# Performance work log

Hardware: AMD Instinct MI355X
Metric: run time of the kernel (lower is better)

Reference implementation:

```python
import jax, jax.numpy as jnp
import numpy as np

L, D, H, DK, DV, VOCAB, PAD = 6, 512, 8, 64, 64, 10000, 0
B, S, NR = 32, 64, 196

def setup_inputs() -> dict:
    key = jax.random.key(0)
    ks = jax.random.split(key, 16)
    sd = 0.02
    emb = jax.random.normal(ks[0], (VOCAB, D), jnp.float32) * sd
    emb = emb.at[PAD].set(0.0)  # padding_idx row is zero in torch Embedding
    def w(k, shape):
        return jax.random.normal(k, shape, jnp.float32) * sd
    return {
        "x": jax.random.randint(ks[1], (B, S), 0, VOCAB),
        "K": jax.random.normal(ks[2], (B, NR, D), jnp.float32),
        "V": jax.random.normal(ks[3], (B, NR, D), jnp.float32),
        "g": jax.random.normal(ks[4], (B, D), jnp.float32),
        "batch_size": B,
        "emb": emb,
        "Wq_s": w(ks[5], (L, D, H * DK)),
        "Wk_s": w(ks[6], (L, D, H * DK)),
        "Wv_s": w(ks[7], (L, D, H * DV)),
        "Wo_s": w(ks[8], (L, H * DV, D)),
        "Wq_c": w(ks[9], (L, D, H * DK)),
        "Wg_c": w(ks[10], (L, D, H * DK)),
        "Wk_c": w(ks[11], (L, D, H * DK)),
        "Wv_c": w(ks[12], (L, D, H * DV)),
        "Wo_c": w(ks[13], (L, H * DV, D)),
        "Wf": w(ks[14], (D, VOCAB)),
        "bf": jnp.zeros((VOCAB,), jnp.float32),
    }

def positional_encoding(seq_len, d_model):
    pos = jnp.arange(seq_len, dtype=jnp.float32)[:, None]          # [S,1]
    j = jnp.arange(d_model // 2, dtype=jnp.float32)[None, :]       # [1,D/2]
    ang = pos / jnp.power(10000.0, 2.0 * j / d_model)              # [S,D/2]
    pe = jnp.stack([jnp.sin(ang), jnp.cos(ang)], axis=-1)          # [S,D/2,2]
    return pe.reshape(seq_len, d_model)

def attend(q, k, v, mask):
    # q:[B,Sq,H,DK] k:[B,Sk,H,DK] v:[B,Sk,H,DV]
    scores = jnp.einsum('bqhd,bkhd->bhqk', q, k) / jnp.sqrt(jnp.float32(DK))
    if mask is not None:
        scores = jnp.where(mask[None, None], scores, jnp.finfo(scores.dtype).min)
    attn = jax.nn.softmax(scores, axis=-1)
    return jnp.einsum('bhqk,bkhd->bqhd', attn, v)

def reference(x, K, V, g, batch_size, emb, Wq_s, Wk_s, Wv_s, Wo_s,
              Wq_c, Wg_c, Wk_c, Wv_c, Wo_c, Wf, bf):
    b, s = x.shape
    out = emb[x] + positional_encoding(s, D)[None]                 # [B,S,D]
    mask = jnp.tril(jnp.ones((s, s), bool))                        # causal: True = attend
    for l in range(L):
        # masked multi-head self-attention
        q = (out @ Wq_s[l]).reshape(b, s, H, DK)
        k = (out @ Wk_s[l]).reshape(b, s, H, DK)
        v = (out @ Wv_s[l]).reshape(b, s, H, DV)
        out = attend(q, k, v, mask).reshape(b, s, H * DV) @ Wo_s[l]
        # global-adaptive cross-attention: query conditioned on global feature g
        q = (out @ Wq_c[l] + (g @ Wg_c[l])[:, None, :]).reshape(b, s, H, DK)
        kk = (K @ Wk_c[l]).reshape(b, NR, H, DK)
        vv = (V @ Wv_c[l]).reshape(b, NR, H, DV)
        out = attend(q, kk, vv, None).reshape(b, s, H * DV) @ Wo_c[l]
    return jax.nn.softmax(out @ Wf + bf, axis=-1)                  # [B,S,VOCAB]
```

## Files before the change

kernel.cpp:

```cpp
#include <hip/hip_runtime.h>
#include <math.h>


#define S2 (512*512)
typedef unsigned short ushort_t;
typedef unsigned int u32;
typedef __attribute__((ext_vector_type(8))) short short8;
typedef __attribute__((ext_vector_type(4))) float f32x4;

__device__ __forceinline__ ushort_t f2b(float f) {
    union { float f; u32 u; } v; v.f = f;
    u32 r = (v.u + 0x7fffu + ((v.u >> 16) & 1u)) >> 16;
    return (ushort_t)r;
}
__device__ __forceinline__ float b2f(ushort_t u) {
    union { u32 u; float f; } v; v.u = ((u32)u) << 16; return v.f;
}
__device__ __forceinline__ void glds16(const void* g, void* l) {
    __builtin_amdgcn_global_load_lds((const __attribute__((address_space(1))) u32*)g,
                                     (__attribute__((address_space(3))) u32*)l,
                                     16, 0, 0);
}
__device__ __forceinline__ f32x4 mfma16(short8 a, short8 b, f32x4 c) {
    return __builtin_amdgcn_mfma_f32_16x16x32_bf16(a, b, c, 0, 0, 0);
}

__device__ __forceinline__ void tile128(
    const ushort_t* __restrict__ A, const ushort_t* __restrict__ B,
    ushort_t* __restrict__ Cp, int N, int K, const float* __restrict__ biasc,
    int m0, int n0, ushort_t* As, ushort_t* Bs, ushort_t* Cs)
{
    int t = threadIdx.x;
    int sr = t >> 2, sk = (t & 3) * 8;
    int wv = t >> 6, lane = t & 63;
    int wr = (wv >> 1) * 64, wc = (wv & 1) * 64;
    int lr = lane & 15, lq = lane >> 4;

    f32x4 acc[4][4];
#pragma unroll
    for (int i = 0; i < 4; ++i)
#pragma unroll
        for (int j = 0; j < 4; ++j) acc[i][j] = (f32x4){0.f, 0.f, 0.f, 0.f};

    for (int k0 = 0; k0 < K; k0 += 32) {
        glds16(A + (long)(m0 + sr) * K + k0 + sk,      (void*)(As + t * 8));
        glds16(A + (long)(m0 + sr + 64) * K + k0 + sk, (void*)(As + (t + 256) * 8));
        glds16(B + (long)(n0 + sr) * K + k0 + sk,      (void*)(Bs + t * 8));
        glds16(B + (long)(n0 + sr + 64) * K + k0 + sk, (void*)(Bs + (t + 256) * 8));
        __syncthreads();
        short8 af[4], bfr[4];
#pragma unroll
        for (int i = 0; i < 4; ++i)
            af[i] = *(const short8*)&As[(wr + i * 16 + lr) * 32 + lq * 8];
#pragma unroll
        for (int j = 0; j < 4; ++j)
            bfr[j] = *(const short8*)&Bs[(wc + j * 16 + lr) * 32 + lq * 8];
#pragma unroll
        for (int i = 0; i < 4; ++i)
#pragma unroll
            for (int j = 0; j < 4; ++j)
                acc[i][j] = mfma16(af[i], bfr[j], acc[i][j]);
        __syncthreads();
    }

    ushort_t* Cw = Cs + wv * 16 * 80;
#pragma unroll
    for (int i = 0; i < 4; ++i) {
#pragma unroll
        for (int j = 0; j < 4; ++j) {
            int colg = n0 + wc + j * 16 + lr;
            float bb = (biasc && colg < N) ? biasc[colg] : 0.f;
#pragma unroll
            for (int r = 0; r < 4; ++r)
                Cw[(lq * 4 + r) * 80 + j * 16 + lr] = f2b(acc[i][j][r] + bb);
        }
        __syncthreads();
#pragma unroll
        for (int rr = 0; rr < 2; ++rr) {
            int c = lane + 64 * rr;
            int row = c >> 3, g8 = c & 7;
            uint4 u = *(const uint4*)&Cw[row * 80 + g8 * 8];
            int colg = n0 + wc + g8 * 8;
            int rowg = m0 + wr + i * 16 + row;
            if (colg < N) *(uint4*)&Cp[(long)rowg * N + colg] = u;
        }
        __syncthreads();
    }
}

__global__ __launch_bounds__(256) void gemm_bt(
    const ushort_t* __restrict__ A, const ushort_t* __restrict__ B,
    ushort_t* __restrict__ C, int N, int K, const float* __restrict__ biasc)
{
    __shared__ ushort_t As[128 * 32], Bs[128 * 32];
    __shared__ __align__(16) ushort_t Cs[4 * 16 * 80];
    tile128(A, B, C, N, K, biasc, blockIdx.y * 128, blockIdx.x * 128, As, Bs, Cs);
}

__global__ __launch_bounds__(256) void fusew(
    const ushort_t* __restrict__ W8t, const ushort_t* __restrict__ Wo_sp,
    const ushort_t* __restrict__ Wo_cp, ushort_t* __restrict__ Fqc_t,
    ushort_t* __restrict__ Fqkv_t)
{
    __shared__ ushort_t As[128 * 32], Bs[128 * 32];
    __shared__ __align__(16) ushort_t Cs[4 * 16 * 80];
    int z = blockIdx.z;
    const ushort_t *A, *B; ushort_t* C;
    if (z < 6)      { A = W8t + (long)(24 + z) * S2; B = Wo_sp + (long)z * S2; C = Fqc_t + (long)z * S2; }
    else { int zz = z - 6, l = zz / 3, m = zz % 3;
           A = W8t + (long)(m * 6 + l + 1) * S2; B = Wo_cp + (long)l * S2; C = Fqkv_t + (long)zz * S2; }
    tile128(A, B, C, 512, 512, nullptr, blockIdx.y * 128, blockIdx.x * 128, As, Bs, Cs);
}

__global__ __launch_bounds__(256) void kcv_gemm(
    const ushort_t* __restrict__ Kb, const ushort_t* __restrict__ Vb,
    const ushort_t* __restrict__ W8t, ushort_t* __restrict__ kcv)
{
    __shared__ ushort_t As[128 * 32], Bs[128 * 32];
    __shared__ __align__(16) ushort_t Cs[4 * 16 * 80];
    int z = blockIdx.z, l = z >> 1, isv = z & 1;
    const ushort_t* A = isv ? Vb : Kb;
    const ushort_t* B = W8t + (long)(30 + isv * 6 + l) * S2;
    ushort_t* C = kcv + (long)z * 3211264;
    tile128(A, B, C, 512, 512, nullptr, blockIdx.y * 128, blockIdx.x * 128, As, Bs, Cs);
}

__global__ __launch_bounds__(256) void prep(
    const int* __restrict__ x, const float* __restrict__ emb,
    const float* __restrict__ Wq_s, const float* __restrict__ Wk_s,
    const float* __restrict__ Wv_s, const float* __restrict__ Wo_s,
    const float* __restrict__ Wq_c, const float* __restrict__ Wg_c,
    const float* __restrict__ Wk_c, const float* __restrict__ Wv_c,
    const float* __restrict__ Wo_c, const float* __restrict__ Wf,
    const float* __restrict__ Kin, const float* __restrict__ Vin,
    const float* __restrict__ g,
    ushort_t* __restrict__ W8t, ushort_t* __restrict__ Wf_t,
    ushort_t* __restrict__ Wo_sp, ushort_t* __restrict__ Wo_cp,
    ushort_t* __restrict__ K_bf, ushort_t* __restrict__ V_bf,
    ushort_t* __restrict__ act0, float* __restrict__ gq)
{
    __shared__ float tile[2][64][65];
    int bid = blockIdx.x, t = threadIdx.x;
    if (bid < 1536) {
        int mat = bid >> 5, wsel = mat / 6, l = mat % 6;
        const float* src = (wsel == 0) ? Wq_s : (wsel == 1) ? Wk_s : (wsel == 2) ? Wv_s :
                           (wsel == 3) ? Wo_s : (wsel == 4) ? Wq_c : (wsel == 5) ? Wk_c :
                           (wsel == 6) ? Wv_c : Wo_c;
        src += (long)l * S2;
        ushort_t* dst = W8t + (long)mat * S2;
        ushort_t* plain = (wsel == 3) ? Wo_sp + (long)l * S2
                        : (wsel == 7) ? Wo_cp + (long)l * S2 : nullptr;
        int within = bid & 31;
        int n0 = (within & 7) * 64, kb = (within >> 3) * 128;
        int r0 = t >> 4, c4 = (t & 15) * 4;
        float4 v[2][4];
#pragma unroll
        for (int h2 = 0; h2 < 2; ++h2)
#pragma unroll
            for (int p = 0; p < 4; ++p)
                v[h2][p] = *(const float4*)(src + (long)(kb + h2 * 64 + p * 16 + r0) * 512 + n0 + c4);
#pragma unroll
        for (int h2 = 0; h2 < 2; ++h2)
#pragma unroll
            for (int p = 0; p < 4; ++p) {
                int r = p * 16 + r0;
                tile[h2][c4 + 0][r] = v[h2][p].x; tile[h2][c4 + 1][r] = v[h2][p].y;
                tile[h2][c4 + 2][r] = v[h2][p].z; tile[h2][c4 + 3][r] = v[h2][p].w;
            }
        if (plain) {
#pragma unroll
            for (int h2 = 0; h2 < 2; ++h2)
#pragma unroll
                for (int p = 0; p < 4; ++p) {
                    ushort4 w;
                    w.x = f2b(v[h2][p].x); w.y = f2b(v[h2][p].y);
                    w.z = f2b(v[h2][p].z); w.w = f2b(v[h2][p].w);
                    *(ushort4*)(plain + (long)(kb + h2 * 64 + p * 16 + r0) * 512 + n0 + c4) = w;
                }
        }
        __syncthreads();
#pragma unroll
        for (int h2 = 0; h2 < 2; ++h2)
#pragma unroll
            for (int q = 0; q < 2; ++q) {
                int nl = q * 32 + (t >> 3), k8 = (t & 7) * 8;
                short8 o;
#pragma unroll
                for (int u = 0; u < 8; ++u) o[u] = (short)f2b(tile[h2][nl][k8 + u]);
                *(short8*)(dst + (long)(n0 + nl) * 512 + kb + h2 * 64 + k8) = o;
            }
    } else if (bid < 2168) {
        int id = bid - 1536;
        int n0 = (id % 158) * 64, kb = (id / 158) * 128;
        int r0 = t >> 4, c4 = (t & 15) * 4;
        int n = n0 + c4;
        float4 v[2][4];
#pragma unroll
        for (int h2 = 0; h2 < 2; ++h2)
#pragma unroll
            for (int p = 0; p < 4; ++p) {
                const float* row = Wf + (long)(kb + h2 * 64 + p * 16 + r0) * 10000;
                float4 w;
                if (n + 3 < 10000) {
                    w = *(const float4*)(row + n);
                } else {
                    w.x = (n + 0 < 10000) ? row[n + 0] : 0.f;
                    w.y = (n + 1 < 10000) ? row[n + 1] : 0.f;
                    w.z = (n + 2 < 10000) ? row[n + 2] : 0.f;
                    w.w = (n + 3 < 10000) ? row[n + 3] : 0.f;
                }
                v[h2][p] = w;
            }
#pragma unroll
        for (int h2 = 0; h2 < 2; ++h2)
#pragma unroll
            for (int p = 0; p < 4; ++p) {
                int r = p * 16 + r0;
                tile[h2][c4 + 0][r] = v[h2][p].x; tile[h2][c4 + 1][r] = v[h2][p].y;
                tile[h2][c4 + 2][r] = v[h2][p].z; tile[h2][c4 + 3][r] = v[h2][p].w;
            }
        __syncthreads();
#pragma unroll
        for (int h2 = 0; h2 < 2; ++h2)
#pragma unroll
            for (int q = 0; q < 2; ++q) {
                int nl = q * 32 + (t >> 3), k8 = (t & 7) * 8;
                short8 o;
#pragma unroll
                for (int u = 0; u < 8; ++u) o[u] = (short)f2b(tile[h2][nl][k8 + u]);
                *(short8*)(Wf_t + (long)(n0 + nl) * 512 + kb + h2 * 64 + k8) = o;
            }
    } else if (bid < 2952) {
        int sec = bid - 2168;
        const float* s; ushort_t* o; long fbase;
        if (sec < 392) { s = Kin; o = K_bf; fbase = (long)sec * 2048; }
        else           { s = Vin; o = V_bf; fbase = (long)(sec - 392) * 2048; }
        float4 v[8];
#pragma unroll
        for (int u = 0; u < 8; ++u)
            v[u] = *(const float4*)(s + 4 * (fbase + t + 256 * u));
#pragma unroll
        for (int u = 0; u < 8; ++u) {
            long fi = fbase + t + 256 * u;
            ushort4 w;
            w.x = f2b(v[u].x); w.y = f2b(v[u].y); w.z = f2b(v[u].z); w.w = f2b(v[u].w);
            *(ushort4*)(o + 4 * fi) = w;
        }
    } else if (bid < 3464) {
        long i = (long)(bid - 2952) * 2048 + t * 8;
        long tok = i >> 9;
        int d8 = (int)(i & 511);
        int s = (int)(tok & 63);
        int id = x[tok];
        const float* erow = emb + (long)id * 512 + d8;
        float4 e0 = *(const float4*)(erow);
        float4 e1 = *(const float4*)(erow + 4);
        float ev[8] = {e0.x, e0.y, e0.z, e0.w, e1.x, e1.y, e1.z, e1.w};
        int j0 = d8 >> 1;
        float sf = (float)s;
        short8 o;
#pragma unroll
        for (int u = 0; u < 4; ++u) {
            float invf = expf(-0.035977892f * (float)(j0 + u));
            float ang = sf * invf;
            o[2 * u]     = (short)f2b(ev[2 * u]     + sinf(ang));
            o[2 * u + 1] = (short)f2b(ev[2 * u + 1] + cosf(ang));
        }
        *(short8*)(act0 + i) = o;
    } else {
        __shared__ float gs[512];
        int id = bid - 3464;
        int lb = id >> 1, half = id & 1;
        int l = lb >> 5, b = lb & 31;
        for (int i = t; i < 512; i += 256) gs[i] = g[b * 512 + i];
        __syncthreads();
        int o = half * 256 + t;
        const float* wcol = Wg_c + (long)l * S2 + o;
        float acc = 0.f;
#pragma unroll 8
        for (int i = 0; i < 512; ++i) acc += gs[i] * wcol[(long)i * 512];
        gq[((long)l * 32 + b) * 512 + o] = acc;
    }
}

__global__ __launch_bounds__(256, 1) void layer_self(
    const ushort_t* __restrict__ act,
    const ushort_t* __restrict__ Wq, const ushort_t* __restrict__ Wk,
    const ushort_t* __restrict__ Wv, ushort_t* __restrict__ attnout)
{
    __shared__ __align__(16) char smem[111616];
    ushort_t* Wst = (ushort_t*)smem;
    ushort_t* Qs  = (ushort_t*)(smem + 66560);
    ushort_t* Ks  = (ushort_t*)(smem + 75776);
    ushort_t* Vt  = (ushort_t*)(smem + 84992);
    float*    Ss  = (float*)(smem + 94208);

    int b = blockIdx.x >> 3, h = blockIdx.x & 7;
    int t = threadIdx.x, wv = t >> 6, lane = t & 63;
    int lr = lane & 15, lq = lane >> 4;
    const ushort_t* actb = act + (long)b * 64 * 512;

    for (int mat = 0; mat < 3; ++mat) {
        const ushort_t* W = ((mat == 0) ? Wq : (mat == 1) ? Wk : Wv) + h * 64 * 512;
        __syncthreads();
#pragma unroll
        for (int i = 0; i < 16; ++i) {
            int row = i * 4 + wv;
            glds16(W + row * 512 + lane * 8, Wst + row * 520 + lane * 8);
        }
        __syncthreads();
        f32x4 acc[4];
#pragma unroll
        for (int j = 0; j < 4; ++j) acc[j] = (f32x4){0.f, 0.f, 0.f, 0.f};
        const ushort_t* arow = actb + (wv * 16 + lr) * 512;
#pragma unroll 4
        for (int k = 0; k < 16; ++k) {
            short8 a = *(const short8*)(arow + k * 32 + lq * 8);
#pragma unroll
            for (int j = 0; j < 4; ++j) {
                short8 bb = *(const short8*)&Wst[(j * 16 + lr) * 520 + k * 32 + lq * 8];
                acc[j] = mfma16(a, bb, acc[j]);
            }
        }
        if (mat == 2) {
#pragma unroll
            for (int j = 0; j < 4; ++j)
#pragma unroll
                for (int r = 0; r < 4; ++r)
                    Vt[(j * 16 + lr) * 72 + wv * 16 + lq * 4 + r] = f2b(acc[j][r]);
        } else {
            ushort_t* Dst = (mat == 0) ? Qs : Ks;
#pragma unroll
            for (int j = 0; j < 4; ++j)
#pragma unroll
                for (int r = 0; r < 4; ++r)
                    Dst[(wv * 16 + lq * 4 + r) * 72 + j * 16 + lr] = f2b(acc[j][r]);
        }
    }
    __syncthreads();

    f32x4 sc[4];
#pragma unroll
    for (int j = 0; j < 4; ++j) sc[j] = (f32x4){0.f, 0.f, 0.f, 0.f};
#pragma unroll
    for (int k2 = 0; k2 < 2; ++k2) {
        short8 a = *(const short8*)&Qs[(wv * 16 + lr) * 72 + k2 * 32 + lq * 8];
#pragma unroll
        for (int j = 0; j < 4; ++j) {
            short8 bb = *(const short8*)&Ks[(j * 16 + lr) * 72 + k2 * 32 + lq * 8];
            sc[j] = mfma16(a, bb, sc[j]);
        }
    }
#pragma unroll
    for (int j = 0; j < 4; ++j)
#pragma unroll
        for (int r = 0; r < 4; ++r)
            Ss[(wv * 16 + lq * 4 + r) * 68 + j * 16 + lr] = sc[j][r];
    __syncthreads();

    for (int rr = 0; rr < 16; ++rr) {
        int r = wv * 16 + rr;
        float sv = (lane <= r) ? Ss[r * 68 + lane] * 0.125f : -INFINITY;
        float m = sv;
        for (int off = 32; off; off >>= 1) m = fmaxf(m, __shfl_xor(m, off));
        float p = __expf(sv - m);
        float su = p;
        for (int off = 32; off; off >>= 1) su += __shfl_xor(su, off);
        Qs[r * 72 + lane] = f2b(p / su);
    }
    __syncthreads();

    f32x4 ov[4];
#pragma unroll
    for (int j = 0; j < 4; ++j) ov[j] = (f32x4){0.f, 0.f, 0.f, 0.f};
#pragma unroll
    for (int k2 = 0; k2 < 2; ++k2) {
        short8 a = *(const short8*)&Qs[(wv * 16 + lr) * 72 + k2 * 32 + lq * 8];
#pragma unroll
        for (int j = 0; j < 4; ++j) {
            short8 bb = *(const short8*)&Vt[(j * 16 + lr) * 72 + k2 * 32 + lq * 8];
            ov[j] = mfma16(a, bb, ov[j]);
        }
    }
    long obase = ((long)b * 64) * 512 + h * 64;
#pragma unroll
    for (int j = 0; j < 4; ++j)
#pragma unroll
        for (int r = 0; r < 4; ++r)
            attnout[obase + (long)(wv * 16 + lq * 4 + r) * 512 + j * 16 + lr] = f2b(ov[j][r]);
}

__global__ __launch_bounds__(256, 1) void layer_cross(
    const ushort_t* __restrict__ attnout, const ushort_t* __restrict__ Kb,
    const ushort_t* __restrict__ Vb, const ushort_t* __restrict__ Fqc,
    const ushort_t* __restrict__ Wkc, const ushort_t* __restrict__ Wvc,
    const float* __restrict__ gql, ushort_t* __restrict__ crossout)
{
    __shared__ __align__(16) char smem[134400];
    ushort_t* Wst = (ushort_t*)smem;
    float*    Ss  = (float*)smem;
    ushort_t* Qs  = (ushort_t*)(smem + 66560);
    ushort_t* Kc  = (ushort_t*)(smem + 75776);
    ushort_t* Pb  = Kc;
    ushort_t* Vt  = (ushort_t*)(smem + 105728);

    int b = blockIdx.x >> 3, h = blockIdx.x & 7;
    int t = threadIdx.x, wv = t >> 6, lane = t & 63;
    int lr = lane & 15, lq = lane >> 4;
    const ushort_t* atb = attnout + (long)b * 64 * 512;
    const ushort_t* Kbb = Kb + (long)b * 196 * 512;
    const ushort_t* Vbb = Vb + (long)b * 196 * 512;

    {
        const ushort_t* W = Fqc + h * 64 * 512;
#pragma unroll
        for (int i = 0; i < 16; ++i) {
            int row = i * 4 + wv;
            glds16(W + row * 512 + lane * 8, Wst + row * 520 + lane * 8);
        }
        __syncthreads();
        f32x4 acc[4];
#pragma unroll
        for (int j = 0; j < 4; ++j) acc[j] = (f32x4){0.f, 0.f, 0.f, 0.f};
        const ushort_t* arow = atb + (wv * 16 + lr) * 512;
#pragma unroll 4
        for (int k = 0; k < 16; ++k) {
            short8 a = *(const short8*)(arow + k * 32 + lq * 8);
#pragma unroll
            for (int j = 0; j < 4; ++j) {
                short8 bb = *(const short8*)&Wst[(j * 16 + lr) * 520 + k * 32 + lq * 8];
                acc[j] = mfma16(a, bb, acc[j]);
            }
        }
#pragma unroll
        for (int j = 0; j < 4; ++j)
#pragma unroll
            for (int r = 0; r < 4; ++r) {
                int col = j * 16 + lr;
                Qs[(wv * 16 + lq * 4 + r) * 72 + col] =
                    f2b(acc[j][r] + gql[b * 512 + h * 64 + col]);
            }
    }
#pragma unroll
    for (int mat = 0; mat < 2; ++mat) {
        const ushort_t* W = ((mat == 0) ? Wkc : Wvc) + h * 64 * 512;
        const ushort_t* Src = (mat == 0) ? Kbb : Vbb;
        __syncthreads();
#pragma unroll
        for (int i = 0; i < 16; ++i) {
            int row = i * 4 + wv;
            glds16(W + row * 512 + lane * 8, Wst + row * 520 + lane * 8);
        }
        __syncthreads();
        for (int rt = wv; rt < 13; rt += 4) {
            f32x4 acc[4];
#pragma unroll
            for (int j = 0; j < 4; ++j) acc[j] = (f32x4){0.f, 0.f, 0.f, 0.f};
            const ushort_t* arow = Src + (long)(rt * 16 + lr) * 512;
#pragma unroll 4
            for (int k = 0; k < 16; ++k) {
                short8 a = *(const short8*)(arow + k * 32 + lq * 8);
#pragma unroll
                for (int j = 0; j < 4; ++j) {
                    short8 bb = *(const short8*)&Wst[(j * 16 + lr) * 520 + k * 32 + lq * 8];
                    acc[j] = mfma16(a, bb, acc[j]);
                }
            }
            if (mat == 0) {
#pragma unroll
                for (int j = 0; j < 4; ++j)
#pragma unroll
                    for (int r = 0; r < 4; ++r)
                        Kc[(rt * 16 + lq * 4 + r) * 72 + j * 16 + lr] = f2b(acc[j][r]);
            } else {
#pragma unroll
                for (int j = 0; j < 4; ++j)
#pragma unroll
                    for (int r = 0; r < 4; ++r)
                        Vt[(j * 16 + lr) * 224 + rt * 16 + lq * 4 + r] = f2b(acc[j][r]);
            }
        }
    }
    __syncthreads();
    for (int e = t; e < 64 * 28; e += 256) Vt[(e / 28) * 224 + 196 + (e % 28)] = 0;

    f32x4 sc[13];
#pragma unroll
    for (int ct = 0; ct < 13; ++ct) sc[ct] = (f32x4){0.f, 0.f, 0.f, 0.f};
#pragma unroll
    for (int k2 = 0; k2 < 2; ++k2) {
        short8 a = *(const short8*)&Qs[(wv * 16 + lr) * 72 + k2 * 32 + lq * 8];
#pragma unroll
        for (int ct = 0; ct < 13; ++ct) {
            short8 bb = *(const short8*)&Kc[(ct * 16 + lr) * 72 + k2 * 32 + lq * 8];
            sc[ct] = mfma16(a, bb, sc[ct]);
        }
    }
#pragma unroll
    for (int ct = 0; ct < 13; ++ct)
#pragma unroll
        for (int r = 0; r < 4; ++r)
            Ss[(wv * 16 + lq * 4 + r) * 216 + ct * 16 + lr] = sc[ct][r];
    __syncthreads();

    for (int rr = 0; rr < 16; ++rr) {
        int r = wv * 16 + rr;
        float v0 = Ss[r * 216 + lane] * 0.125f;
        float v1 = Ss[r * 216 + 64 + lane] * 0.125f;
        float v2 = Ss[r * 216 + 128 + lane] * 0.125f;
        float v3 = (lane < 4) ? Ss[r * 216 + 192 + lane] * 0.125f : -INFINITY;
        float m = fmaxf(fmaxf(v0, v1), fmaxf(v2, v3));
        for (int off = 32; off; off >>= 1) m = fmaxf(m, __shfl_xor(m, off));
        float e0 = __expf(v0 - m), e1 = __expf(v1 - m), e2 = __expf(v2 - m);
        float e3 = (lane < 4) ? __expf(v3 - m) : 0.f;
        float su = e0 + e1 + e2 + e3;
        for (int off = 32; off; off >>= 1) su += __shfl_xor(su, off);
        float inv = 1.f / su;
        Pb[r * 224 + lane]       = f2b(e0 * inv);
        Pb[r * 224 + 64 + lane]  = f2b(e1 * inv);
        Pb[r * 224 + 128 + lane] = f2b(e2 * inv);
        if (lane < 4)  Pb[r * 224 + 192 + lane] = f2b(e3 * inv);
        if (lane < 28) Pb[r * 224 + 196 + lane] = 0;
    }
    __syncthreads();

    f32x4 ov[4];
#pragma unroll
    for (int j = 0; j < 4; ++j) ov[j] = (f32x4){0.f, 0.f, 0.f, 0.f};
#pragma unroll
    for (int k2 = 0; k2 < 7; ++k2) {
        short8 a = *(const short8*)&Pb[(wv * 16 + lr) * 224 + k2 * 32 + lq * 8];
#pragma unroll
        for (int j = 0; j < 4; ++j) {
            short8 bb = *(const short8*)&Vt[(j * 16 + lr) * 224 + k2 * 32 + lq * 8];
            ov[j] = mfma16(a, bb, ov[j]);
        }
    }
    long obase = ((long)b * 64) * 512 + h * 64;
#pragma unroll
    for (int j = 0; j < 4; ++j)
#pragma unroll
        for (int r = 0; r < 4; ++r)
            crossout[obase + (long)(wv * 16 + lq * 4 + r) * 512 + j * 16 + lr] = f2b(ov[j][r]);
}

__global__ __launch_bounds__(256, 1) void layer_cross_pre(
    const ushort_t* __restrict__ attnout, const ushort_t* __restrict__ kcl,
    const ushort_t* __restrict__ vcl, const ushort_t* __restrict__ Fqc,
    const float* __restrict__ gql, ushort_t* __restrict__ crossout)
{
    __shared__ __align__(16) char smem[134400];
    ushort_t* Wst = (ushort_t*)smem;
    float*    Ss  = (float*)smem;
    ushort_t* Qs  = (ushort_t*)(smem + 66560);
    ushort_t* Kc  = (ushort_t*)(smem + 75776);
    ushort_t* Pb  = Kc;
    ushort_t* Vt  = (ushort_t*)(smem + 105728);

    int b = blockIdx.x >> 3, h = blockIdx.x & 7;
    int t = threadIdx.x, wv = t >> 6, lane = t & 63;
    int lr = lane & 15, lq = lane >> 4;
    const ushort_t* atb = attnout + (long)b * 64 * 512;

    {
        const ushort_t* W = Fqc + h * 64 * 512;
#pragma unroll
        for (int i = 0; i < 16; ++i) {
            int row = i * 4 + wv;
            glds16(W + row * 512 + lane * 8, Wst + row * 520 + lane * 8);
        }
        __syncthreads();
        f32x4 acc[4];
#pragma unroll
        for (int j = 0; j < 4; ++j) acc[j] = (f32x4){0.f, 0.f, 0.f, 0.f};
        const ushort_t* arow = atb + (wv * 16 + lr) * 512;
#pragma unroll 4
        for (int k = 0; k < 16; ++k) {
            short8 a = *(const short8*)(arow + k * 32 + lq * 8);
#pragma unroll
            for (int j = 0; j < 4; ++j) {
                short8 bb = *(const short8*)&Wst[(j * 16 + lr) * 520 + k * 32 + lq * 8];
                acc[j] = mfma16(a, bb, acc[j]);
            }
        }
#pragma unroll
        for (int j = 0; j < 4; ++j)
#pragma unroll
            for (int r = 0; r < 4; ++r) {
                int col = j * 16 + lr;
                Qs[(wv * 16 + lq * 4 + r) * 72 + col] =
                    f2b(acc[j][r] + gql[b * 512 + h * 64 + col]);
            }
    }

    {
        const ushort_t* kr = kcl + ((long)b * 196) * 512 + h * 64;
        for (int idx = t; idx < 208 * 8; idx += 256) {
            int key = idx >> 3, d8 = (idx & 7) * 8;
            short8 v = (short8){0, 0, 0, 0, 0, 0, 0, 0};
            if (key < 196) v = *(const short8*)(kr + (long)key * 512 + d8);
            *(short8*)&Kc[key * 72 + d8] = v;
        }
        const ushort_t* vrp = vcl + ((long)b * 196) * 512 + h * 64;
        for (int idx = t; idx < 196 * 8; idx += 256) {
            int key = idx >> 3, d8 = (idx & 7) * 8;
            short8 v = *(const short8*)(vrp + (long)key * 512 + d8);
#pragma unroll
            for (int u = 0; u < 8; ++u) Vt[(d8 + u) * 224 + key] = v[u];
        }
        for (int e = t; e < 64 * 28; e += 256) Vt[(e / 28) * 224 + 196 + (e % 28)] = 0;
    }
    __syncthreads();

    f32x4 sc[13];
#pragma unroll
    for (int ct = 0; ct < 13; ++ct) sc[ct] = (f32x4){0.f, 0.f, 0.f, 0.f};
#pragma unroll
    for (int k2 = 0; k2 < 2; ++k2) {
        short8 a = *(const short8*)&Qs[(wv * 16 + lr) * 72 + k2 * 32 + lq * 8];
#pragma unroll
        for (int ct = 0; ct < 13; ++ct) {
            short8 bb = *(const short8*)&Kc[(ct * 16 + lr) * 72 + k2 * 32 + lq * 8];
            sc[ct] = mfma16(a, bb, sc[ct]);
        }
    }
#pragma unroll
    for (int ct = 0; ct < 13; ++ct)
#pragma unroll
        for (int r = 0; r < 4; ++r)
            Ss[(wv * 16 + lq * 4 + r) * 216 + ct * 16 + lr] = sc[ct][r];
    __syncthreads();

    for (int rr = 0; rr < 16; ++rr) {
        int r = wv * 16 + rr;
        float v0 = Ss[r * 216 + lane] * 0.125f;
        float v1 = Ss[r * 216 + 64 + lane] * 0.125f;
        float v2 = Ss[r * 216 + 128 + lane] * 0.125f;
        float v3 = (lane < 4) ? Ss[r * 216 + 192 + lane] * 0.125f : -INFINITY;
        float m = fmaxf(fmaxf(v0, v1), fmaxf(v2, v3));
        for (int off = 32; off; off >>= 1) m = fmaxf(m, __shfl_xor(m, off));
        float e0 = __expf(v0 - m), e1 = __expf(v1 - m), e2 = __expf(v2 - m);
        float e3 = (lane < 4) ? __expf(v3 - m) : 0.f;
        float su = e0 + e1 + e2 + e3;
        for (int off = 32; off; off >>= 1) su += __shfl_xor(su, off);
        float inv = 1.f / su;
        Pb[r * 224 + lane]       = f2b(e0 * inv);
        Pb[r * 224 + 64 + lane]  = f2b(e1 * inv);
        Pb[r * 224 + 128 + lane] = f2b(e2 * inv);
        if (lane < 4)  Pb[r * 224 + 192 + lane] = f2b(e3 * inv);
        if (lane < 28) Pb[r * 224 + 196 + lane] = 0;
    }
    __syncthreads();

    f32x4 ov[4];
#pragma unroll
    for (int j = 0; j < 4; ++j) ov[j] = (f32x4){0.f, 0.f, 0.f, 0.f};
#pragma unroll
    for (int k2 = 0; k2 < 7; ++k2) {
        short8 a = *(const short8*)&Pb[(wv * 16 + lr) * 224 + k2 * 32 + lq * 8];
#pragma unroll
        for (int j = 0; j < 4; ++j) {
            short8 bb = *(const short8*)&Vt[(j * 16 + lr) * 224 + k2 * 32 + lq * 8];
            ov[j] = mfma16(a, bb, ov[j]);
        }
    }
    long obase = ((long)b * 64) * 512 + h * 64;
#pragma unroll
    for (int j = 0; j < 4; ++j)
#pragma unroll
        for (int r = 0; r < 4; ++r)
            crossout[obase + (long)(wv * 16 + lq * 4 + r) * 512 + j * 16 + lr] = f2b(ov[j][r]);
}

__global__ __launch_bounds__(256) void softmax_bf(const ushort_t* __restrict__ lg,
                                                  float* __restrict__ out)
{
    __shared__ float red[8];
    long row = blockIdx.x;
    const ushort_t* p = lg + row * 10000L;
    float* po = out + row * 10000L;
    int t = threadIdx.x;
    int w = t >> 6, lane = t & 63;
    float vals[40];
    float mx = -INFINITY;
#pragma unroll
    for (int i = 0; i < 5; ++i) {
        int vi = t + (i << 8);
        if (vi < 1250) {
            short8 v = *(const short8*)(p + vi * 8);
#pragma unroll
            for (int u = 0; u < 8; ++u) {
                float f = b2f((ushort_t)v[u]);
                vals[i * 8 + u] = f;
                mx = fmaxf(mx, f);
            }
        } else {
#pragma unroll
            for (int u = 0; u < 8; ++u) vals[i * 8 + u] = -INFINITY;
        }
    }
    for (int off = 32; off; off >>= 1) mx = fmaxf(mx, __shfl_xor(mx, off));
    if (lane == 0) red[w] = mx;
    __syncthreads();
    mx = fmaxf(fmaxf(red[0], red[1]), fmaxf(red[2], red[3]));
    float s = 0.f;
#pragma unroll
    for (int ii = 0; ii < 40; ++ii) {
        float e = __expf(vals[ii] - mx);
        vals[ii] = e;
        s += e;
    }
    for (int off = 32; off; off >>= 1) s += __shfl_xor(s, off);
    if (lane == 0) red[4 + w] = s;
    __syncthreads();
    s = red[4] + red[5] + red[6] + red[7];
    float inv = 1.0f / s;
#pragma unroll
    for (int i = 0; i < 5; ++i) {
        int vi = t + (i << 8);
        if (vi < 1250) {
#pragma unroll
            for (int u4 = 0; u4 < 2; ++u4) {
                float4 o;
                o.x = vals[i * 8 + u4 * 4 + 0] * inv;
                o.y = vals[i * 8 + u4 * 4 + 1] * inv;
                o.z = vals[i * 8 + u4 * 4 + 2] * inv;
                o.w = vals[i * 8 + u4 * 4 + 3] * inv;
                *(float4*)(po + vi * 8 + u4 * 4) = o;
            }
        }
    }
}

extern "C" void kernel_launch(void* const* d_in, const int* in_sizes, int n_in,
                              void* d_out, int out_size, void* d_ws, size_t ws_size,
                              hipStream_t stream)
{
    const int*   x    = (const int*)d_in[0];
    const float* Kin  = (const float*)d_in[1];
    const float* Vin  = (const float*)d_in[2];
    const float* g    = (const float*)d_in[3];
    const float* emb  = (const float*)d_in[5];
    const float* Wq_s = (const float*)d_in[6];
    const float* Wk_s = (const float*)d_in[7];
    const float* Wv_s = (const float*)d_in[8];
    const float* Wo_s = (const float*)d_in[9];
    const float* Wq_c = (const float*)d_in[10];
    const float* Wg_c = (const float*)d_in[11];
    const float* Wk_c = (const float*)d_in[12];
    const float* Wv_c = (const float*)d_in[13];
    const float* Wo_c = (const float*)d_in[14];
    const float* Wf   = (const float*)d_in[15];
    const float* bf   = (const float*)d_in[16];
    float* out = (float*)d_out;

    float* gq = (float*)d_ws;
    ushort_t* act0     = (ushort_t*)(gq + 98304);
    ushort_t* crossout = act0 + 1048576;
    ushort_t* attnout  = crossout + 1048576;
    ushort_t* K_bf     = attnout + 1048576;
    ushort_t* V_bf     = K_bf + 3211264;
    ushort_t* W8t      = V_bf + 3211264;
    ushort_t* Wf_t     = W8t + 48L * S2;
    ushort_t* Wo_sp    = Wf_t + 5177344;
    ushort_t* Wo_cp    = Wo_sp + 6L * S2;
    ushort_t* Fqc_t    = Wo_cp + 6L * S2;
    ushort_t* Fqkv_t   = Fqc_t + 6L * S2;
    ushort_t* Wfin_t   = Fqkv_t + 15L * S2;
    ushort_t* kcv      = Wfin_t + 5177344;
    ushort_t* logits   = W8t;

    int use_pre = (ws_size >= 159776768ULL) ? 1 : 0;

    prep<<<3848, 256, 0, stream>>>(x, emb, Wq_s, Wk_s, Wv_s, Wo_s, Wq_c, Wg_c,
                                   Wk_c, Wv_c, Wo_c, Wf, Kin, Vin, g,
                                   W8t, Wf_t, Wo_sp, Wo_cp, K_bf, V_bf, act0, gq);
    fusew<<<dim3(4, 4, 21), 256, 0, stream>>>(W8t, Wo_sp, Wo_cp, Fqc_t, Fqkv_t);
    gemm_bt<<<dim3(4, 79, 1), 256, 0, stream>>>(Wf_t, Wo_cp + 5L * S2, Wfin_t,
                                                512, 512, nullptr);
    if (use_pre)
        kcv_gemm<<<dim3(4, 49, 12), 256, 0, stream>>>(K_bf, V_bf, W8t, kcv);

    for (int l = 0; l < 6; ++l) {
        const ushort_t *A, *Bq, *Bk, *Bv;
        if (l == 0) {
            A = act0;
            Bq = W8t + 0L * 6 * S2; Bk = W8t + 1L * 6 * S2; Bv = W8t + 2L * 6 * S2;
        } else {
            A = crossout;
            Bq = Fqkv_t + (long)((l - 1) * 3) * S2;
            Bk = Bq + S2; Bv = Bq + 2 * S2;
        }
        layer_self<<<256, 256, 0, stream>>>(A, Bq, Bk, Bv, attnout);
        if (use_pre)
            layer_cross_pre<<<256, 256, 0, stream>>>(attnout,
                                                     kcv + (long)(l * 2) * 3211264,
                                                     kcv + (long)(l * 2 + 1) * 3211264,
                                                     Fqc_t + (long)l * S2,
                                                     gq + (long)l * 16384, crossout);
        else
            layer_cross<<<256, 256, 0, stream>>>(attnout, K_bf, V_bf,
                                                 Fqc_t + (long)l * S2,
                                                 W8t + (long)(5 * 6 + l) * S2,
                                                 W8t + (long)(6 * 6 + l) * S2,
                                                 gq + (long)l * 16384, crossout);
    }

    gemm_bt<<<dim3(79, 16, 1), 256, 0, stream>>>(crossout, Wfin_t, logits,
                                                 10000, 512, bf);
    softmax_bf<<<2048, 256, 0, stream>>>(logits, out);
}
```

Before: 655.1 us.

## Read weights directly from global and do softmax in registers to raise occupancy

Removes the LDS staging of the per-head weight slice in the self-attention and cross-attention pre kernels, so the B operand is read straight from global memory. The score tile is no longer spilled to a float LDS buffer; softmax runs on the MFMA accumulators using 16-lane shuffles. This shrinks shared memory enough to allow two blocks per CU (launch bounds raised to 2) and drops several barriers. The cost is uncoalesced, cache-dependent global reads of the weights inside the MFMA loop and more register pressure from the register-resident softmax.

```diff
diff --git a/kernel.cpp b/kernel.cpp
--- a/kernel.cpp
+++ b/kernel.cpp
@@ -283,42 +283,34 @@
     }
 }
 
-__global__ __launch_bounds__(256, 1) void layer_self(
+__global__ __launch_bounds__(256, 2) void layer_self(
     const ushort_t* __restrict__ act,
     const ushort_t* __restrict__ Wq, const ushort_t* __restrict__ Wk,
     const ushort_t* __restrict__ Wv, ushort_t* __restrict__ attnout)
 {
-    __shared__ __align__(16) char smem[111616];
-    ushort_t* Wst = (ushort_t*)smem;
-    ushort_t* Qs  = (ushort_t*)(smem + 66560);
-    ushort_t* Ks  = (ushort_t*)(smem + 75776);
-    ushort_t* Vt  = (ushort_t*)(smem + 84992);
-    float*    Ss  = (float*)(smem + 94208);
+    __shared__ __align__(16) char smem[27648];
+    ushort_t* Qs = (ushort_t*)smem;
+    ushort_t* Ks = (ushort_t*)(smem + 9216);
+    ushort_t* Vt = (ushort_t*)(smem + 18432);
 
     int b = blockIdx.x >> 3, h = blockIdx.x & 7;
     int t = threadIdx.x, wv = t >> 6, lane = t & 63;
     int lr = lane & 15, lq = lane >> 4;
     const ushort_t* actb = act + (long)b * 64 * 512;
-
+    const ushort_t* arow = actb + (wv * 16 + lr) * 512;
+
+#pragma unroll
     for (int mat = 0; mat < 3; ++mat) {
         const ushort_t* W = ((mat == 0) ? Wq : (mat == 1) ? Wk : Wv) + h * 64 * 512;
-        __syncthreads();
-#pragma unroll
-        for (int i = 0; i < 16; ++i) {
-            int row = i * 4 + wv;
-            glds16(W + row * 512 + lane * 8, Wst + row * 520 + lane * 8);
-        }
-        __syncthreads();
         f32x4 acc[4];
 #pragma unroll
         for (int j = 0; j < 4; ++j) acc[j] = (f32x4){0.f, 0.f, 0.f, 0.f};
-        const ushort_t* arow = actb + (wv * 16 + lr) * 512;
 #pragma unroll 4
         for (int k = 0; k < 16; ++k) {
             short8 a = *(const short8*)(arow + k * 32 + lq * 8);
 #pragma unroll
             for (int j = 0; j < 4; ++j) {
-                short8 bb = *(const short8*)&Wst[(j * 16 + lr) * 520 + k * 32 + lq * 8];
+                short8 bb = *(const short8*)(W + (j * 16 + lr) * 512 + k * 32 + lq * 8);
                 acc[j] = mfma16(a, bb, acc[j]);
             }
         }
@@ -351,25 +343,26 @@
             sc[j] = mfma16(a, bb, sc[j]);
         }
     }
-#pragma unroll
-    for (int j = 0; j < 4; ++j)
-#pragma unroll
-        for (int r = 0; r < 4; ++r)
-            Ss[(wv * 16 + lq * 4 + r) * 68 + j * 16 + lr] = sc[j][r];
-    __syncthreads();
-
-    for (int rr = 0; rr < 16; ++rr) {
-        int r = wv * 16 + rr;
-        float sv = (lane <= r) ? Ss[r * 68 + lane] * 0.125f : -INFINITY;
-        float m = sv;
-        for (int off = 32; off; off >>= 1) m = fmaxf(m, __shfl_xor(m, off));
-        float p = __expf(sv - m);
-        float su = p;
-        for (int off = 32; off; off >>= 1) su += __shfl_xor(su, off);
-        Qs[r * 72 + lane] = f2b(p / su);
-    }
-    __syncthreads();
-
+
+#pragma unroll
+    for (int r = 0; r < 4; ++r) {
+        int row = wv * 16 + lq * 4 + r;
+        float v[4], m = -INFINITY;
+#pragma unroll
+        for (int j = 0; j < 4; ++j) {
+            v[j] = (j * 16 + lr <= row) ? sc[j][r] * 0.125f : -INFINITY;
+            m = fmaxf(m, v[j]);
+        }
+        for (int off = 8; off; off >>= 1) m = fmaxf(m, __shfl_xor(m, off));
+        float su = 0.f;
+#pragma unroll
+        for (int j = 0; j < 4; ++j) { v[j] = __expf(v[j] - m); su += v[j]; }
+        for (int off = 8; off; off >>= 1) su += __shfl_xor(su, off);
+        float inv = 1.f / su;
+#pragma unroll
+        for (int j = 0; j < 4; ++j)
+            Qs[row * 72 + j * 16 + lr] = f2b(v[j] * inv);
+    }
     f32x4 ov[4];
 #pragma unroll
     for (int j = 0; j < 4; ++j) ov[j] = (f32x4){0.f, 0.f, 0.f, 0.f};
@@ -544,18 +537,16 @@
             crossout[obase + (long)(wv * 16 + lq * 4 + r) * 512 + j * 16 + lr] = f2b(ov[j][r]);
 }
 
-__global__ __launch_bounds__(256, 1) void layer_cross_pre(
+__global__ __launch_bounds__(256, 2) void layer_cross_pre(
     const ushort_t* __restrict__ attnout, const ushort_t* __restrict__ kcl,
     const ushort_t* __restrict__ vcl, const ushort_t* __restrict__ Fqc,
     const float* __restrict__ gql, ushort_t* __restrict__ crossout)
 {
-    __shared__ __align__(16) char smem[134400];
-    ushort_t* Wst = (ushort_t*)smem;
-    float*    Ss  = (float*)smem;
-    ushort_t* Qs  = (ushort_t*)(smem + 66560);
-    ushort_t* Kc  = (ushort_t*)(smem + 75776);
-    ushort_t* Pb  = Kc;
-    ushort_t* Vt  = (ushort_t*)(smem + 105728);
+    __shared__ __align__(16) char smem[67840];
+    ushort_t* Qs = (ushort_t*)smem;
+    ushort_t* Kc = (ushort_t*)(smem + 9216);
+    ushort_t* Pb = Kc;
+    ushort_t* Vt = (ushort_t*)(smem + 39168);
 
     int b = blockIdx.x >> 3, h = blockIdx.x & 7;
     int t = threadIdx.x, wv = t >> 6, lane = t & 63;
@@ -564,12 +555,6 @@
 
     {
         const ushort_t* W = Fqc + h * 64 * 512;
-#pragma unroll
-        for (int i = 0; i < 16; ++i) {
-            int row = i * 4 + wv;
-            glds16(W + row * 512 + lane * 8, Wst + row * 520 + lane * 8);
-        }
-        __syncthreads();
         f32x4 acc[4];
 #pragma unroll
         for (int j = 0; j < 4; ++j) acc[j] = (f32x4){0.f, 0.f, 0.f, 0.f};
@@ -579,7 +564,7 @@
             short8 a = *(const short8*)(arow + k * 32 + lq * 8);
 #pragma unroll
             for (int j = 0; j < 4; ++j) {
-                short8 bb = *(const short8*)&Wst[(j * 16 + lr) * 520 + k * 32 + lq * 8];
+                short8 bb = *(const short8*)(W + (j * 16 + lr) * 512 + k * 32 + lq * 8);
                 acc[j] = mfma16(a, bb, acc[j]);
             }
         }
@@ -624,33 +609,30 @@
             sc[ct] = mfma16(a, bb, sc[ct]);
         }
     }
-#pragma unroll
-    for (int ct = 0; ct < 13; ++ct)
-#pragma unroll
-        for (int r = 0; r < 4; ++r)
-            Ss[(wv * 16 + lq * 4 + r) * 216 + ct * 16 + lr] = sc[ct][r];
     __syncthreads();
 
-    for (int rr = 0; rr < 16; ++rr) {
-        int r = wv * 16 + rr;
-        float v0 = Ss[r * 216 + lane] * 0.125f;
-        float v1 = Ss[r * 216 + 64 + lane] * 0.125f;
-        float v2 = Ss[r * 216 + 128 + lane] * 0.125f;
-        float v3 = (lane < 4) ? Ss[r * 216 + 192 + lane] * 0.125f : -INFINITY;
-        float m = fmaxf(fmaxf(v0, v1), fmaxf(v2, v3));
-        for (int off = 32; off; off >>= 1) m = fmaxf(m, __shfl_xor(m, off));
-        float e0 = __expf(v0 - m), e1 = __expf(v1 - m), e2 = __expf(v2 - m);
-        float e3 = (lane < 4) ? __expf(v3 - m) : 0.f;
-        float su = e0 + e1 + e2 + e3;
-        for (int off = 32; off; off >>= 1) su += __shfl_xor(su, off);
+#pragma unroll
+    for (int r = 0; r < 4; ++r) {
+        int row = wv * 16 + lq * 4 + r;
+        float v[13], m = -INFINITY;
+#pragma unroll
+        for (int ct = 0; ct < 13; ++ct) {
+            v[ct] = (ct * 16 + lr < 196) ? sc[ct][r] * 0.125f : -INFINITY;
+            m = fmaxf(m, v[ct]);
+        }
+        for (int off = 8; off; off >>= 1) m = fmaxf(m, __shfl_xor(m, off));
+        float su = 0.f;
+#pragma unroll
+        for (int ct = 0; ct < 13; ++ct) { v[ct] = __expf(v[ct] - m); su += v[ct]; }
+        for (int off = 8; off; off >>= 1) su += __shfl_xor(su, off);
         float inv = 1.f / su;
-        Pb[r * 224 + lane]       = f2b(e0 * inv);
-        Pb[r * 224 + 64 + lane]  = f2b(e1 * inv);
-        Pb[r * 224 + 128 + lane] = f2b(e2 * inv);
-        if (lane < 4)  Pb[r * 224 + 192 + lane] = f2b(e3 * inv);
-        if (lane < 28) Pb[r * 224 + 196 + lane] = 0;
-    }
-    __syncthreads();
+#pragma unroll
+        for (int ct = 0; ct < 13; ++ct) {
+            int col = ct * 16 + lr;
+            Pb[row * 224 + col] = (col < 196) ? f2b(v[ct] * inv) : (ushort_t)0;
+        }
+        Pb[row * 224 + 208 + lr] = 0;
+    }
 
     f32x4 ov[4];
 #pragma unroll
```

Result: slower. 706.9 us (+7.9%).
